# Kernel optimization log

Measured on AMD Instinct MI355X. Metric: run time of the kernel, lower is better.

The kernel has to match this reference:

```python
import jax, jax.numpy as jnp
import numpy as np

B, N, V, H, R, A, IN, K = 64, 512, 64, 512, 4, 18, 128, 32
EPS = 1e-8


def setup_inputs() -> dict:
    key = jax.random.key(0)
    ks = jax.random.split(key, 20)
    g = lambda i, shape, s=1.0: jax.random.normal(ks[i], shape, jnp.float32) * s
    u = lambda i, shape: jax.random.uniform(ks[i], shape, dtype=jnp.float32)
    cin = IN + R * V
    return dict(
        x=g(0, (B, IN)),
        h=g(1, (B, H), 0.1),
        c=g(2, (B, H), 0.1),
        memory=g(3, (B, N, V), 0.1),
        read_weights=u(4, (B, R, N)),
        write_weights=u(5, (B, N)),
        usage=u(6, (B, N)),
        link_matrix=u(7, (B, N, N)) * 0.01,
        precedence_weights=u(8, (B, N)),
        W_ih=g(9, (4 * H, cin), 0.05), W_hh=g(10, (4 * H, H), 0.05),
        b_ih=jnp.zeros(4 * H, jnp.float32), b_hh=jnp.zeros(4 * H, jnp.float32),
        W_read=g(11, (R, V + 4, H), 0.05), b_read=jnp.zeros((R, V + 4), jnp.float32),
        W_write=g(12, (3 * V + 3, H), 0.05), b_write=jnp.zeros(3 * V + 3, jnp.float32),
        W_pol=g(13, (A, H), 0.05), b_pol=jnp.zeros(A, jnp.float32),
        W_val=g(14, (1, H), 0.05), b_val=jnp.zeros(1, jnp.float32),
    )


def reference(x, h, c, memory, read_weights, write_weights, usage, link_matrix,
              precedence_weights, W_ih, W_hh, b_ih, b_hh, W_read, b_read,
              W_write, b_write, W_pol, b_pol, W_val, b_val):
    # ---- read heads (vectorized over R) ----
    ro = jnp.einsum('roh,bh->bro', W_read, h) + b_read            # [B,R,V+4]
    rkey = ro[..., :V]
    rbeta = jax.nn.softplus(ro[..., V])                           # [B,R]
    rpi = jax.nn.softmax(ro[..., V + 1:V + 4], axis=-1)           # backward/content/forward gates
    mem_norm = jnp.maximum(jnp.linalg.norm(memory, axis=-1), EPS)  # [B,N]
    key_norm = jnp.maximum(jnp.linalg.norm(rkey, axis=-1), EPS)    # [B,R]
    sim = jnp.einsum('bnv,brv->brn', memory, rkey) / (mem_norm[:, None, :] * key_norm[..., None])
    scores = rbeta[..., None] * sim                                # [B,R,N]
    kth = jax.lax.top_k(scores, K)[0][..., -1:]                    # sparse top-k mask
    cw = jax.nn.softmax(jnp.where(scores >= kth, scores, -jnp.inf), axis=-1)
    fw = jnp.einsum('bnm,brm->brn', link_matrix, read_weights)     # forward weighting L w
    bw = jnp.einsum('bmn,brm->brn', link_matrix, read_weights)     # backward weighting L^T w
    w_r = rpi[..., 0:1] * bw + rpi[..., 1:2] * cw + rpi[..., 2:3] * fw  # [B,R,N]
    rvec = jnp.einsum('brn,bnv->brv', w_r, memory).reshape(B, R * V)
    # ---- LSTM controller (torch LSTMCell gate order i,f,g,o) ----
    gates = jnp.concatenate([x, rvec], -1) @ W_ih.T + h @ W_hh.T + b_ih + b_hh
    i_g, f_g, g_g, o_g = jnp.split(gates, 4, axis=-1)
    c_new = jax.nn.sigmoid(f_g) * c + jax.nn.sigmoid(i_g) * jnp.tanh(g_g)
    h_new = jax.nn.sigmoid(o_g) * jnp.tanh(c_new)
    # ---- write head ----
    wo = h_new @ W_write.T + b_write                               # [B,3V+3]
    wkey = wo[:, :V]
    erase = jax.nn.sigmoid(wo[:, V:2 * V])
    add = jnp.tanh(wo[:, 2 * V:3 * V])
    wbeta = jax.nn.softplus(wo[:, 3 * V])
    g_a = jax.nn.sigmoid(wo[:, 3 * V + 1])
    g_w = jax.nn.sigmoid(wo[:, 3 * V + 2])
    wkey_norm = jnp.maximum(jnp.linalg.norm(wkey, axis=-1), EPS)
    wsim = jnp.einsum('bnv,bv->bn', memory, wkey) / (mem_norm * wkey_norm[:, None])
    cw_w = jax.nn.softmax(wbeta[:, None] * wsim, axis=-1)
    # allocation weighting from sorted usage (DNC Eq. 1)
    idx = jnp.argsort(usage, axis=-1)
    u_sorted = jnp.take_along_axis(usage, idx, -1)
    prod_prev = jnp.concatenate([jnp.ones((B, 1), usage.dtype), jnp.cumprod(u_sorted, -1)[:, :-1]], -1)
    a_sorted = (1.0 - u_sorted) * prod_prev
    alloc = jnp.take_along_axis(a_sorted, jnp.argsort(idx, -1), -1)
    write_w = g_w[:, None] * (g_a[:, None] * alloc + (1.0 - g_a)[:, None] * cw_w)  # [B,N]
    # ---- memory erase/add ----
    mem_new = memory * (1.0 - write_w[:, :, None] * erase[:, None, :]) + write_w[:, :, None] * add[:, None, :]
    # ---- usage (psi detached as in torch.no_grad) ----
    psi = jax.lax.stop_gradient(jnp.prod(1.0 - w_r, axis=1))
    usage_new = (usage + write_weights - usage * write_weights) * psi
    # ---- link matrix + precedence ----
    ws = jnp.sum(write_w, -1, keepdims=True)
    prec_new = (1.0 - ws) * precedence_weights + write_w
    decay = (1.0 - write_w[:, :, None]) * (1.0 - write_w[:, None, :])
    link_new = decay * link_matrix + write_w[:, :, None] * precedence_weights[:, None, :]
    link_new = link_new * (1.0 - jnp.eye(N, dtype=link_new.dtype))
    # ---- actor/critic heads ----
    logits = h_new @ W_pol.T + b_pol
    value = h_new @ W_val.T + b_val
    return (logits, value, h_new, c_new, mem_new, w_r, write_w, usage_new, link_new, prec_new)
```

## Files before the change

### kernel.cpp

```cpp
#include <hip/hip_runtime.h>
#include <math.h>

constexpr int Bb = 64, Nn = 512, Vv = 64, Hh = 512, Rr = 4, Aa = 18, INp = 128, KTOP = 32;
constexpr int CIN = 384;
constexpr int WOUT = 195;
#define EPSf 1e-8f

__device__ __forceinline__ float sigmoidf(float x){ return 1.f/(1.f+expf(-x)); }
__device__ __forceinline__ float softplusf(float x){ return (x>20.f)? x : log1pf(expf(x)); }
__device__ __forceinline__ float wave_reduce(float v){
  #pragma unroll
  for(int o=32;o>0;o>>=1) v += __shfl_down(v, o, 64);
  return v;
}
__device__ __forceinline__ unsigned f2ord(float f){
  unsigned u = __float_as_uint(f);
  return (u & 0x80000000u) ? ~u : (u | 0x80000000u);
}
__device__ __forceinline__ const float* wrow_sel(int d, const float* Ww, const float* Wp, const float* Wv){
  return (d < WOUT) ? Ww + (size_t)d*Hh : ((d < WOUT+Aa) ? Wp + (size_t)(d-WOUT)*Hh : Wv);
}

__global__ void k_stage1(const float* __restrict__ link, const float* __restrict__ rw,
                         const float* __restrict__ Wr, const float* __restrict__ brd,
                         const float* __restrict__ h, const float* __restrict__ mem,
                         float* __restrict__ fw, float* __restrict__ bwpart,
                         float* __restrict__ rvec, float* __restrict__ rp,
                         float* __restrict__ cw) {
  __shared__ __align__(16) float smem[8192];
  if (blockIdx.x < 1024) {
    float4 (*bl4)[4][128] = reinterpret_cast<float4 (*)[4][128]>(smem);
    if (blockIdx.x < 64) rvec[blockIdx.x*256 + threadIdx.x] = 0.f;
    int b  = blockIdx.x >> 4;
    int ch = blockIdx.x & 15;
    int wv = threadIdx.x >> 6, lane = threadIdx.x & 63;
    const float* rwb = rw + b*Rr*Nn;
    const float4* rw4 = (const float4*)rwb;
    float4 rwv4[4][2];
    #pragma unroll
    for (int r = 0; r < 4; ++r) {
      rwv4[r][0] = rw4[r*128 + lane];
      rwv4[r][1] = rw4[r*128 + 64 + lane];
    }
    float4 bwacc[2][4];
    #pragma unroll
    for (int t = 0; t < 2; ++t)
      #pragma unroll
      for (int r = 0; r < 4; ++r) bwacc[t][r] = make_float4(0.f,0.f,0.f,0.f);
    const float4* lb4 = (const float4*)(link + (size_t)b*Nn*Nn);
    int n0 = ch*32 + wv*8;
    #pragma unroll 2
    for (int i = 0; i < 8; ++i) {
      int n = n0 + i;
      float4 A = lb4[n*128 + lane];
      float4 Bv = lb4[n*128 + 64 + lane];
      float s0 = rwb[n], s1 = rwb[512+n], s2 = rwb[1024+n], s3 = rwb[1536+n];
      float f0 = A.x*rwv4[0][0].x + A.y*rwv4[0][0].y + A.z*rwv4[0][0].z + A.w*rwv4[0][0].w
               + Bv.x*rwv4[0][1].x + Bv.y*rwv4[0][1].y + Bv.z*rwv4[0][1].z + Bv.w*rwv4[0][1].w;
      float f1 = A.x*rwv4[1][0].x + A.y*rwv4[1][0].y + A.z*rwv4[1][0].z + A.w*rwv4[1][0].w
               + Bv.x*rwv4[1][1].x + Bv.y*rwv4[1][1].y + Bv.z*rwv4[1][1].z + Bv.w*rwv4[1][1].w;
      float f2 = A.x*rwv4[2][0].x + A.y*rwv4[2][0].y + A.z*rwv4[2][0].z + A.w*rwv4[2][0].w
               + Bv.x*rwv4[2][1].x + Bv.y*rwv4[2][1].y + Bv.z*rwv4[2][1].z + Bv.w*rwv4[2][1].w;
      float f3 = A.x*rwv4[3][0].x + A.y*rwv4[3][0].y + A.z*rwv4[3][0].z + A.w*rwv4[3][0].w
               + Bv.x*rwv4[3][1].x + Bv.y*rwv4[3][1].y + Bv.z*rwv4[3][1].z + Bv.w*rwv4[3][1].w;
      bwacc[0][0].x += A.x*s0; bwacc[0][0].y += A.y*s0; bwacc[0][0].z += A.z*s0; bwacc[0][0].w += A.w*s0;
      bwacc[0][1].x += A.x*s1; bwacc[0][1].y += A.y*s1; bwacc[0][1].z += A.z*s1; bwacc[0][1].w += A.w*s1;
      bwacc[0][2].x += A.x*s2; bwacc[0][2].y += A.y*s2; bwacc[0][2].z += A.z*s2; bwacc[0][2].w += A.w*s2;
      bwacc[0][3].x += A.x*s3; bwacc[0][3].y += A.y*s3; bwacc[0][3].z += A.z*s3; bwacc[0][3].w += A.w*s3;
      bwacc[1][0].x += Bv.x*s0; bwacc[1][0].y += Bv.y*s0; bwacc[1][0].z += Bv.z*s0; bwacc[1][0].w += Bv.w*s0;
      bwacc[1][1].x += Bv.x*s1; bwacc[1][1].y += Bv.y*s1; bwacc[1][1].z += Bv.z*s1; bwacc[1][1].w += Bv.w*s1;
      bwacc[1][2].x += Bv.x*s2; bwacc[1][2].y += Bv.y*s2; bwacc[1][2].z += Bv.z*s2; bwacc[1][2].w += Bv.w*s2;
      bwacc[1][3].x += Bv.x*s3; bwacc[1][3].y += Bv.y*s3; bwacc[1][3].z += Bv.z*s3; bwacc[1][3].w += Bv.w*s3;
      #pragma unroll
      for (int o = 32; o > 0; o >>= 1) {
        f0 += __shfl_down(f0,o,64); f1 += __shfl_down(f1,o,64);
        f2 += __shfl_down(f2,o,64); f3 += __shfl_down(f3,o,64);
      }
      if (lane == 0) {
        fw[(b*Rr+0)*Nn+n] = f0; fw[(b*Rr+1)*Nn+n] = f1;
        fw[(b*Rr+2)*Nn+n] = f2; fw[(b*Rr+3)*Nn+n] = f3;
      }
    }
    #pragma unroll
    for (int r = 0; r < 4; ++r) {
      bl4[wv][r][lane]      = bwacc[0][r];
      bl4[wv][r][64 + lane] = bwacc[1][r];
    }
    __syncthreads();
    int tid = threadIdx.x;
    float4* bwp4 = (float4*)bwpart;
    #pragma unroll
    for (int q = 0; q < 2; ++q) {
      int fid = q*256 + tid;
      int r = fid >> 7, j4 = fid & 127;
      float4 a = bl4[0][r][j4], bb = bl4[1][r][j4], cc = bl4[2][r][j4], dd = bl4[3][r][j4];
      float4 v;
      v.x = a.x+bb.x+cc.x+dd.x; v.y = a.y+bb.y+cc.y+dd.y;
      v.z = a.z+bb.z+cc.z+dd.z; v.w = a.w+bb.w+cc.w+dd.w;
      bwp4[((size_t)(ch*Bb + b)*Rr + r)*128 + j4] = v;
    }
  } else {
    float* sh  = smem;
    float* sro = smem + 512;
    unsigned long long* sk = (unsigned long long*)(smem + 592);
    float* sred = smem + 1616;
    float* skv  = smem + 1620;
    int blk = blockIdx.x - 1024;
    int b = blk >> 2, r = blk & 3;
    int tid = threadIdx.x;
    int wv = tid >> 6, lane = tid & 63;
    const float* hb = h + b*Hh;
    for (int i = tid; i < 512; i += 256) sh[i] = hb[i];
    __syncthreads();
    const float* wbase = Wr + (size_t)(r*68)*Hh;
    int pbase = wv*17;
    #pragma unroll
    for (int g = 0; g < 4; ++g) {
      int p = pbase + g*4;
      const float *w0 = wbase + (size_t)p*Hh, *w1 = w0 + Hh, *w2 = w1 + Hh, *w3 = w2 + Hh;
      float a0=0,a1=0,a2=0,a3=0;
      #pragma unroll
      for (int t = 0; t < 8; ++t) {
        int k = lane + 64*t; float hv = sh[k];
        a0 += w0[k]*hv; a1 += w1[k]*hv; a2 += w2[k]*hv; a3 += w3[k]*hv;
      }
      #pragma unroll
      for (int o = 32; o > 0; o >>= 1) {
        a0 += __shfl_down(a0,o,64); a1 += __shfl_down(a1,o,64);
        a2 += __shfl_down(a2,o,64); a3 += __shfl_down(a3,o,64);
      }
      if (lane == 0) {
        sro[p]   = a0 + brd[r*68+p];   sro[p+1] = a1 + brd[r*68+p+1];
        sro[p+2] = a2 + brd[r*68+p+2]; sro[p+3] = a3 + brd[r*68+p+3];
      }
    }
    {
      int p = pbase + 16;
      const float* w0 = wbase + (size_t)p*Hh;
      float a0 = 0.f;
      #pragma unroll
      for (int t = 0; t < 8; ++t) { int k = lane + 64*t; a0 += w0[k]*sh[k]; }
      a0 = wave_reduce(a0);
      if (lane == 0) sro[p] = a0 + brd[r*68+p];
    }
    __syncthreads();
    if (wv == 0) {
      float kv = sro[lane];
      float k2 = wave_reduce(kv*kv);
      if (lane == 0) {
        float rbeta = softplusf(sro[64]);
        float sc = rbeta / fmaxf(sqrtf(k2), EPSf);
        float e0 = sro[65], e1 = sro[66], e2 = sro[67];
        float mm = fmaxf(e0, fmaxf(e1, e2));
        float x0 = expf(e0-mm), x1 = expf(e1-mm), x2 = expf(e2-mm);
        float inv = 1.f/(x0+x1+x2);
        float* rpb = rp + (b*4 + r)*4;
        rpb[0] = sc; rpb[1] = x0*inv; rpb[2] = x1*inv; rpb[3] = x2*inv;
        sro[68] = sc;
      }
    }
    __syncthreads();
    float sc = sro[68];
    const float4* key4 = (const float4*)sro;
    float v0, v1;
    {
      const float4* m4 = (const float4*)(mem + ((size_t)(b*Nn + tid))*Vv);
      float dot=0.f, nrm=0.f;
      #pragma unroll
      for (int i = 0; i < 16; ++i) {
        float4 mv = m4[i]; float4 kk = key4[i];
        dot += mv.x*kk.x + mv.y*kk.y + mv.z*kk.z + mv.w*kk.w;
        nrm += mv.x*mv.x + mv.y*mv.y + mv.z*mv.z + mv.w*mv.w;
      }
      v0 = sc * dot / fmaxf(sqrtf(nrm), EPSf);
    }
    {
      const float4* m4 = (const float4*)(mem + ((size_t)(b*Nn + tid + 256))*Vv);
      float dot=0.f, nrm=0.f;
      #pragma unroll
      for (int i = 0; i < 16; ++i) {
        float4 mv = m4[i]; float4 kk = key4[i];
        dot += mv.x*kk.x + mv.y*kk.y + mv.z*kk.z + mv.w*kk.w;
        nrm += mv.x*mv.x + mv.y*mv.y + mv.z*mv.z + mv.w*mv.w;
      }
      v1 = sc * dot / fmaxf(sqrtf(nrm), EPSf);
    }
    unsigned long long k0 = ((unsigned long long)f2ord(v0) << 32) | (unsigned)(511 - tid);
    unsigned long long k1 = ((unsigned long long)f2ord(v1) << 32) | (unsigned)(255 - tid);
    sk[tid] = k0; sk[tid+256] = k1;
    __syncthreads();
    int c0 = 0, c1 = 0;
    #pragma unroll 8
    for (int j = 0; j < 512; ++j) {
      unsigned long long kj = sk[j];
      c0 += (kj > k0); c1 += (kj > k1);
    }
    if (c0 == KTOP-1) skv[0] = v0;
    if (c1 == KTOP-1) skv[0] = v1;
    if (c0 == 0) skv[1] = v0;
    if (c1 == 0) skv[1] = v1;
    __syncthreads();
    float kth = skv[0], mx = skv[1];
    float e0 = (v0 >= kth) ? expf(v0-mx) : 0.f;
    float e1 = (v1 >= kth) ? expf(v1-mx) : 0.f;
    float s = wave_reduce(e0+e1);
    if (lane == 0) sred[wv] = s;
    __syncthreads();
    float inv = 1.f/(sred[0]+sred[1]+sred[2]+sred[3]);
    int brr = b*4 + r;
    cw[brr*Nn+tid]     = e0*inv;
    cw[brr*Nn+tid+256] = e1*inv;
  }
}

__global__ void k_wrrv(const float* __restrict__ bwpart, const float* __restrict__ cw,
                       const float* __restrict__ fw, const float* __restrict__ rp,
                       const float* __restrict__ usage, const float* __restrict__ wwt,
                       const float* __restrict__ mem,
                       float* __restrict__ out_wr, float* __restrict__ out_usage,
                       float* __restrict__ rvec) {
  __shared__ float swr[4][64];
  int b = blockIdx.x >> 3, ch = blockIdx.x & 7;
  int tid = threadIdx.x;
  int r = tid >> 6, nl = tid & 63;
  int n = ch*64 + nl;
  int brr = b*4 + r;
  float bwv = 0.f;
  #pragma unroll
  for (int chh = 0; chh < 16; ++chh)
    bwv += bwpart[((size_t)(chh*Bb + b)*Rr + r)*Nn + n];
  const float* rpb = rp + brr*4;
  float w = rpb[1]*bwv + rpb[2]*cw[brr*Nn+n] + rpb[3]*fw[brr*Nn+n];
  out_wr[brr*Nn+n] = w;
  swr[r][nl] = w;
  __syncthreads();
  if (tid < 64) {
    int idx = b*Nn + ch*64 + tid;
    float psi = (1.f-swr[0][tid])*(1.f-swr[1][tid])*(1.f-swr[2][tid])*(1.f-swr[3][tid]);
    float u = usage[idx], wt = wwt[idx];
    out_usage[idx] = (u + wt - u*wt) * psi;
  }
  const float* mb = mem + ((size_t)b*Nn + ch*64)*Vv + nl;
  float acc = 0.f;
  #pragma unroll 16
  for (int t = 0; t < 64; ++t) acc += swr[r][t] * mb[t*Vv];
  atomicAdd(&rvec[brr*Vv + nl], acc);
}

__global__ void k_gates_lstm(const float* __restrict__ x, const float* __restrict__ rvec,
                             const float* __restrict__ h, const float* __restrict__ Wih,
                             const float* __restrict__ Whh, const float* __restrict__ bih,
                             const float* __restrict__ bhh, const float* __restrict__ c,
                             float* __restrict__ out_h, float* __restrict__ out_c) {
  int gid = blockIdx.x*4 + (threadIdx.x>>6);
  int lane = threadIdx.x & 63;
  int hh = gid >> 4;
  int bt = gid & 15;
  float acc[4][4] = {};
  #pragma unroll
  for (int t = 0; t < 6; ++t) {
    int k = lane + 64*t;
    float u[4], w[4];
    #pragma unroll
    for (int i = 0; i < 4; ++i) {
      int b = bt*4 + i;
      u[i] = (k < INp) ? x[b*INp + k] : rvec[b*(Rr*Vv) + k - INp];
      w[i] = Wih[(size_t)(i*Hh + hh)*CIN + k];
    }
    #pragma unroll
    for (int g = 0; g < 4; ++g)
      #pragma unroll
      for (int bb = 0; bb < 4; ++bb) acc[g][bb] += w[g]*u[bb];
  }
  #pragma unroll
  for (int t = 0; t < 8; ++t) {
    int k = lane + 64*t;
    float u[4], w[4];
    #pragma unroll
    for (int i = 0; i < 4; ++i) {
      u[i] = h[(bt*4+i)*Hh + k];
      w[i] = Whh[(size_t)(i*Hh + hh)*Hh + k];
    }
    #pragma unroll
    for (int g = 0; g < 4; ++g)
      #pragma unroll
      for (int bb = 0; bb < 4; ++bb) acc[g][bb] += w[g]*u[bb];
  }
  #pragma unroll
  for (int g = 0; g < 4; ++g)
    #pragma unroll
    for (int bb = 0; bb < 4; ++bb) acc[g][bb] = wave_reduce(acc[g][bb]);
  if (lane == 0) {
    float bsum[4];
    #pragma unroll
    for (int g = 0; g < 4; ++g) bsum[g] = bih[g*Hh + hh] + bhh[g*Hh + hh];
    #pragma unroll
    for (int bb = 0; bb < 4; ++bb) {
      int b = bt*4 + bb;
      float ig = sigmoidf(acc[0][bb] + bsum[0]);
      float fg = sigmoidf(acc[1][bb] + bsum[1]);
      float gg = tanhf   (acc[2][bb] + bsum[2]);
      float og = sigmoidf(acc[3][bb] + bsum[3]);
      float cn = fg * c[b*Hh + hh] + ig * gg;
      float hn = og * tanhf(cn);
      out_c[b*Hh + hh] = cn;
      out_h[b*Hh + hh] = hn;
    }
  }
}

__global__ void k_tail(const float* __restrict__ hn, const float* __restrict__ Ww,
                       const float* __restrict__ bw_, const float* __restrict__ Wp,
                       const float* __restrict__ bp, const float* __restrict__ Wv,
                       const float* __restrict__ bv, const float* __restrict__ usage,
                       const float* __restrict__ prec, const float* __restrict__ mem,
                       float* __restrict__ wo, float* __restrict__ out_logits,
                       float* __restrict__ out_value, float* __restrict__ out_ww,
                       float* __restrict__ out_prec) {
  __shared__ __align__(16) float sh[512];
  __shared__ __align__(16) float swo[200];
  __shared__ unsigned long long sk[512];
  __shared__ float su[512];
  __shared__ float cp[512];
  __shared__ float sred[8];
  int b = blockIdx.x, tid = threadIdx.x;
  int wv = tid >> 6, lane = tid & 63;
  const float* hb = hn + b*Hh;
  sh[tid] = hb[tid]; sh[tid+256] = hb[tid+256];
  __syncthreads();
  const float4* sh4 = (const float4*)sh;
  float4 h0 = sh4[lane*2], h1 = sh4[lane*2+1];
  int dbeg = wv*54, dend = (dbeg + 54 < 214) ? dbeg + 54 : 214;
  for (int p = dbeg; p < dend; p += 4) {
    int d1 = (p+1 < 213) ? p+1 : 213, d2 = (p+2 < 213) ? p+2 : 213, d3 = (p+3 < 213) ? p+3 : 213;
    const float4* w04 = (const float4*)wrow_sel(p,  Ww, Wp, Wv);
    const float4* w14 = (const float4*)wrow_sel(d1, Ww, Wp, Wv);
    const float4* w24 = (const float4*)wrow_sel(d2, Ww, Wp, Wv);
    const float4* w34 = (const float4*)wrow_sel(d3, Ww, Wp, Wv);
    float4 A0 = w04[lane*2], B0 = w04[lane*2+1];
    float4 A1 = w14[lane*2], B1 = w14[lane*2+1];
    float4 A2 = w24[lane*2], B2 = w24[lane*2+1];
    float4 A3 = w34[lane*2], B3 = w34[lane*2+1];
    float a0 = A0.x*h0.x + A0.y*h0.y + A0.z*h0.z + A0.w*h0.w
             + B0.x*h1.x + B0.y*h1.y + B0.z*h1.z + B0.w*h1.w;
    float a1 = A1.x*h0.x + A1.y*h0.y + A1.z*h0.z + A1.w*h0.w
             + B1.x*h1.x + B1.y*h1.y + B1.z*h1.z + B1.w*h1.w;
    float a2 = A2.x*h0.x + A2.y*h0.y + A2.z*h0.z + A2.w*h0.w
             + B2.x*h1.x + B2.y*h1.y + B2.z*h1.z + B2.w*h1.w;
    float a3 = A3.x*h0.x + A3.y*h0.y + A3.z*h0.z + A3.w*h0.w
             + B3.x*h1.x + B3.y*h1.y + B3.z*h1.z + B3.w*h1.w;
    #pragma unroll
    for (int o = 32; o > 0; o >>= 1) {
      a0 += __shfl_down(a0,o,64); a1 += __shfl_down(a1,o,64);
      a2 += __shfl_down(a2,o,64); a3 += __shfl_down(a3,o,64);
    }
    if (lane == 0) {
      float av[4] = {a0,a1,a2,a3};
      #pragma unroll
      for (int i = 0; i < 4; ++i) {
        int d = p + i;
        if (d >= dend) break;
        float a = av[i];
        if (d < WOUT)          { float vv = a + bw_[d]; swo[d] = vv; wo[b*WOUT+d] = vv; }
        else if (d < WOUT+Aa)  { out_logits[b*Aa + (d-WOUT)] = a + bp[d-WOUT]; }
        else                   { out_value[b] = a + bv[0]; }
      }
    }
  }
  __syncthreads();
  float wbeta = softplusf(swo[192]);
  const float4* key4 = (const float4*)swo;
  float s0, s1;
  {
    const float4* m4 = (const float4*)(mem + ((size_t)(b*Nn + tid))*Vv);
    float dot=0.f, nrm=0.f, kn=0.f;
    #pragma unroll
    for (int i = 0; i < 16; ++i) {
      float4 mv = m4[i]; float4 kk = key4[i];
      dot += mv.x*kk.x + mv.y*kk.y + mv.z*kk.z + mv.w*kk.w;
      nrm += mv.x*mv.x + mv.y*mv.y + mv.z*mv.z + mv.w*mv.w;
      kn  += kk.x*kk.x + kk.y*kk.y + kk.z*kk.z + kk.w*kk.w;
    }
    s0 = wbeta * dot / (fmaxf(sqrtf(nrm), EPSf) * fmaxf(sqrtf(kn), EPSf));
  }
  {
    const float4* m4 = (const float4*)(mem + ((size_t)(b*Nn + tid + 256))*Vv);
    float dot=0.f, nrm=0.f, kn=0.f;
    #pragma unroll
    for (int i = 0; i < 16; ++i) {
      float4 mv = m4[i]; float4 kk = key4[i];
      dot += mv.x*kk.x + mv.y*kk.y + mv.z*kk.z + mv.w*kk.w;
      nrm += mv.x*mv.x + mv.y*mv.y + mv.z*mv.z + mv.w*mv.w;
      kn  += kk.x*kk.x + kk.y*kk.y + kk.z*kk.z + kk.w*kk.w;
    }
    s1 = wbeta * dot / (fmaxf(sqrtf(nrm), EPSf) * fmaxf(sqrtf(kn), EPSf));
  }
  float u0 = usage[b*Nn+tid], u1 = usage[b*Nn+tid+256];
  unsigned long long k0 = ((unsigned long long)f2ord(u0) << 32) | (unsigned)tid;
  unsigned long long k1 = ((unsigned long long)f2ord(u1) << 32) | (unsigned)(tid+256);
  sk[tid] = k0; sk[tid+256] = k1;
  float mxl = fmaxf(s0, s1);
  #pragma unroll
  for (int o = 32; o > 0; o >>= 1) mxl = fmaxf(mxl, __shfl_down(mxl,o,64));
  if (lane == 0) sred[wv] = mxl;
  __syncthreads();
  float mx = fmaxf(fmaxf(sred[0],sred[1]), fmaxf(sred[2],sred[3]));
  float e0 = expf(s0-mx), e1 = expf(s1-mx);
  float ssum = wave_reduce(e0+e1);
  if (lane == 0) sred[4+wv] = ssum;
  int r0 = 0, r1 = 0;
  #pragma unroll 8
  for (int j = 0; j < 512; ++j) {
    unsigned long long kj = sk[j];
    r0 += (kj < k0); r1 += (kj < k1);
  }
  __syncthreads();
  float cinv = 1.f/(sred[4]+sred[5]+sred[6]+sred[7]);
  float c0 = e0*cinv, c1 = e1*cinv;
  su[r0] = u0; su[r1] = u1;
  __syncthreads();
  cp[tid] = su[tid]; cp[tid+256] = su[tid+256];
  __syncthreads();
  for (int d = 1; d < 512; d <<= 1) {
    float t0 = cp[tid]     * ((tid >= d)     ? cp[tid-d]     : 1.f);
    float t1 = cp[tid+256] * ((tid+256 >= d) ? cp[tid+256-d] : 1.f);
    __syncthreads();
    cp[tid] = t0; cp[tid+256] = t1;
    __syncthreads();
  }
  float pp0 = (r0 == 0) ? 1.f : cp[r0-1];
  float pp1 = (r1 == 0) ? 1.f : cp[r1-1];
  float a0 = (1.f-u0)*pp0, a1 = (1.f-u1)*pp1;
  float ga = sigmoidf(swo[193]);
  float gw = sigmoidf(swo[194]);
  float wv0 = gw * (ga*a0 + (1.f-ga)*c0);
  float wv1 = gw * (ga*a1 + (1.f-ga)*c1);
  out_ww[b*Nn+tid]     = wv0;
  out_ww[b*Nn+tid+256] = wv1;
  float ws_ = wave_reduce(wv0+wv1);
  if (lane == 0) sred[wv] = ws_;
  __syncthreads();
  float wsum = sred[0]+sred[1]+sred[2]+sred[3];
  out_prec[b*Nn+tid]     = (1.f-wsum)*prec[b*Nn+tid]     + wv0;
  out_prec[b*Nn+tid+256] = (1.f-wsum)*prec[b*Nn+tid+256] + wv1;
}

__global__ void k_memlink(const float* __restrict__ link, const float* __restrict__ ww,
                          const float* __restrict__ prec, const float* __restrict__ mem,
                          const float* __restrict__ wo, float* __restrict__ out_link,
                          float* __restrict__ out_mem) {
  int bid = blockIdx.x;
  if (bid < 16384) {
    int idx4 = bid*256 + threadIdx.x;
    int base = idx4*4;
    int b = base >> 18;
    int rem = base & 262143;
    int i = rem >> 9;
    int j0 = rem & 511;
    float wi = ww[b*Nn + i];
    float fi = 1.f - wi;
    float4 lv = *(const float4*)(link + base);
    float4 wj = *(const float4*)(ww + b*Nn + j0);
    float4 pj = *(const float4*)(prec + b*Nn + j0);
    float4 o;
    o.x = fi*(1.f-wj.x)*lv.x + wi*pj.x;
    o.y = fi*(1.f-wj.y)*lv.y + wi*pj.y;
    o.z = fi*(1.f-wj.z)*lv.z + wi*pj.z;
    o.w = fi*(1.f-wj.w)*lv.w + wi*pj.w;
    if (i >= j0 && i < j0+4) {
      if (i == j0) o.x = 0.f;
      else if (i == j0+1) o.y = 0.f;
      else if (i == j0+2) o.z = 0.f;
      else o.w = 0.f;
    }
    *(float4*)(out_link + base) = o;
  } else {
    int idx4 = (bid - 16384)*256 + threadIdx.x;
    int base = idx4*4;
    int b = base >> 15;
    int rem = base & 32767;
    int n = rem >> 6;
    int v0 = rem & 63;
    float w = ww[b*Nn + n];
    const float* wob = wo + b*WOUT;
    float4 m = *(const float4*)(mem + base);
    float4 o;
    float e, a;
    e = sigmoidf(wob[64+v0+0]); a = tanhf(wob[128+v0+0]); o.x = m.x*(1.f-w*e)+w*a;
    e = sigmoidf(wob[64+v0+1]); a = tanhf(wob[128+v0+1]); o.y = m.y*(1.f-w*e)+w*a;
    e = sigmoidf(wob[64+v0+2]); a = tanhf(wob[128+v0+2]); o.z = m.z*(1.f-w*e)+w*a;
    e = sigmoidf(wob[64+v0+3]); a = tanhf(wob[128+v0+3]); o.w = m.w*(1.f-w*e)+w*a;
    *(float4*)(out_mem + base) = o;
  }
}

extern "C" void kernel_launch(void* const* d_in, const int* in_sizes, int n_in,
                              void* d_out, int out_size, void* d_ws, size_t ws_size,
                              hipStream_t stream) {
  const float* x    = (const float*)d_in[0];
  const float* h    = (const float*)d_in[1];
  const float* c    = (const float*)d_in[2];
  const float* mem  = (const float*)d_in[3];
  const float* rw   = (const float*)d_in[4];
  const float* wwt  = (const float*)d_in[5];
  const float* usage= (const float*)d_in[6];
  const float* link = (const float*)d_in[7];
  const float* prec = (const float*)d_in[8];
  const float* Wih  = (const float*)d_in[9];
  const float* Whh  = (const float*)d_in[10];
  const float* bih  = (const float*)d_in[11];
  const float* bhh  = (const float*)d_in[12];
  const float* Wr   = (const float*)d_in[13];
  const float* br   = (const float*)d_in[14];
  const float* Ww   = (const float*)d_in[15];
  const float* bw_  = (const float*)d_in[16];
  const float* Wp   = (const float*)d_in[17];
  const float* bp   = (const float*)d_in[18];
  const float* Wv   = (const float*)d_in[19];
  const float* bv   = (const float*)d_in[20];

  float* out = (float*)d_out;
  float* o_logits = out + 0;
  float* o_value  = out + 1152;
  float* o_h      = out + 1216;
  float* o_c      = out + 33984;
  float* o_mem    = out + 66752;
  float* o_wr     = out + 2163904;
  float* o_ww     = out + 2294976;
  float* o_usage  = out + 2327744;
  float* o_link   = out + 2360512;
  float* o_prec   = out + 19137728;

  float* ws = (float*)d_ws;
  float* ws_rp     = ws;
  float* ws_cw     = ws + 1024;
  float* ws_fw     = ws + 132096;
  float* ws_bwpart = ws + 263168;
  float* ws_rvec   = ws + 2360320;
  float* ws_wo     = ws + 2376704;

  k_stage1     <<<dim3(1280),       dim3(256), 0, stream>>>(link, rw, Wr, br, h, mem, ws_fw, ws_bwpart, ws_rvec, ws_rp, ws_cw);
  k_wrrv       <<<dim3(Bb*8),       dim3(256), 0, stream>>>(ws_bwpart, ws_cw, ws_fw, ws_rp, usage, wwt, mem, o_wr, o_usage, ws_rvec);
  k_gates_lstm <<<dim3(2048),       dim3(256), 0, stream>>>(x, ws_rvec, h, Wih, Whh, bih, bhh, c, o_h, o_c);
  k_tail       <<<dim3(Bb),         dim3(256), 0, stream>>>(o_h, Ww, bw_, Wp, bp, Wv, bv, usage, prec, mem, ws_wo, o_logits, o_value, o_ww, o_prec);
  k_memlink    <<<dim3(16384+2048), dim3(256), 0, stream>>>(link, o_ww, prec, mem, ws_wo, o_link, o_mem);
}
```

Before: 307.3 us.

## Tile link matrix through LDS for forward/backward read weightings

Rewrites the link-matrix part of stage1 so each block loads 64x64 tiles of the link matrix into padded shared memory and computes both L·w (row dot) and Lᵀ·w (column dot) from the tile. Blocks now cover 64-row stripes (8 per batch) instead of 32-row chunks, which halves the partial backward-weight buffer and the reduction work in k_wrrv. It replaces the shuffle reductions and the large per-thread register accumulators with scalar LDS dot products, at the cost of two barriers per tile, scalar LDS stores and fewer blocks (512 versus 1024) to stream the matrix.

Result: faster. 292.5 us (-4.8%).

```diff
diff --git a/kernel.cpp b/kernel.cpp
--- a/kernel.cpp
+++ b/kernel.cpp
@@ -27,85 +27,55 @@
                          float* __restrict__ fw, float* __restrict__ bwpart,
                          float* __restrict__ rvec, float* __restrict__ rp,
                          float* __restrict__ cw) {
-  __shared__ __align__(16) float smem[8192];
-  if (blockIdx.x < 1024) {
-    float4 (*bl4)[4][128] = reinterpret_cast<float4 (*)[4][128]>(smem);
-    if (blockIdx.x < 64) rvec[blockIdx.x*256 + threadIdx.x] = 0.f;
-    int b  = blockIdx.x >> 4;
-    int ch = blockIdx.x & 15;
-    int wv = threadIdx.x >> 6, lane = threadIdx.x & 63;
-    const float* rwb = rw + b*Rr*Nn;
-    const float4* rw4 = (const float4*)rwb;
-    float4 rwv4[4][2];
-    #pragma unroll
-    for (int r = 0; r < 4; ++r) {
-      rwv4[r][0] = rw4[r*128 + lane];
-      rwv4[r][1] = rw4[r*128 + 64 + lane];
-    }
-    float4 bwacc[2][4];
-    #pragma unroll
-    for (int t = 0; t < 2; ++t)
-      #pragma unroll
-      for (int r = 0; r < 4; ++r) bwacc[t][r] = make_float4(0.f,0.f,0.f,0.f);
+  __shared__ __align__(16) float smem[6208];
+  if (blockIdx.x < 512) {
+    float* lds   = smem;
+    float* ldsrw = smem + 4160;
+    int b  = blockIdx.x >> 3;
+    int st = blockIdx.x & 7;
+    int tid = threadIdx.x;
+    {
+      const float4* rw4 = (const float4*)(rw + b*Rr*Nn);
+      float4* lrw4 = (float4*)ldsrw;
+      lrw4[tid] = rw4[tid];
+      lrw4[tid+256] = rw4[tid+256];
+    }
+    if (blockIdx.x < 64) rvec[blockIdx.x*256 + tid] = 0.f;
+    __syncthreads();
+    int row = tid & 63, rr = tid >> 6;
+    float facc = 0.f;
     const float4* lb4 = (const float4*)(link + (size_t)b*Nn*Nn);
-    int n0 = ch*32 + wv*8;
-    #pragma unroll 2
-    for (int i = 0; i < 8; ++i) {
-      int n = n0 + i;
-      float4 A = lb4[n*128 + lane];
-      float4 Bv = lb4[n*128 + 64 + lane];
-      float s0 = rwb[n], s1 = rwb[512+n], s2 = rwb[1024+n], s3 = rwb[1536+n];
-      float f0 = A.x*rwv4[0][0].x + A.y*rwv4[0][0].y + A.z*rwv4[0][0].z + A.w*rwv4[0][0].w
-               + Bv.x*rwv4[0][1].x + Bv.y*rwv4[0][1].y + Bv.z*rwv4[0][1].z + Bv.w*rwv4[0][1].w;
-      float f1 = A.x*rwv4[1][0].x + A.y*rwv4[1][0].y + A.z*rwv4[1][0].z + A.w*rwv4[1][0].w
-               + Bv.x*rwv4[1][1].x + Bv.y*rwv4[1][1].y + Bv.z*rwv4[1][1].z + Bv.w*rwv4[1][1].w;
-      float f2 = A.x*rwv4[2][0].x + A.y*rwv4[2][0].y + A.z*rwv4[2][0].z + A.w*rwv4[2][0].w
-               + Bv.x*rwv4[2][1].x + Bv.y*rwv4[2][1].y + Bv.z*rwv4[2][1].z + Bv.w*rwv4[2][1].w;
-      float f3 = A.x*rwv4[3][0].x + A.y*rwv4[3][0].y + A.z*rwv4[3][0].z + A.w*rwv4[3][0].w
-               + Bv.x*rwv4[3][1].x + Bv.y*rwv4[3][1].y + Bv.z*rwv4[3][1].z + Bv.w*rwv4[3][1].w;
-      bwacc[0][0].x += A.x*s0; bwacc[0][0].y += A.y*s0; bwacc[0][0].z += A.z*s0; bwacc[0][0].w += A.w*s0;
-      bwacc[0][1].x += A.x*s1; bwacc[0][1].y += A.y*s1; bwacc[0][1].z += A.z*s1; bwacc[0][1].w += A.w*s1;
-      bwacc[0][2].x += A.x*s2; bwacc[0][2].y += A.y*s2; bwacc[0][2].z += A.z*s2; bwacc[0][2].w += A.w*s2;
-      bwacc[0][3].x += A.x*s3; bwacc[0][3].y += A.y*s3; bwacc[0][3].z += A.z*s3; bwacc[0][3].w += A.w*s3;
-      bwacc[1][0].x += Bv.x*s0; bwacc[1][0].y += Bv.y*s0; bwacc[1][0].z += Bv.z*s0; bwacc[1][0].w += Bv.w*s0;
-      bwacc[1][1].x += Bv.x*s1; bwacc[1][1].y += Bv.y*s1; bwacc[1][1].z += Bv.z*s1; bwacc[1][1].w += Bv.w*s1;
-      bwacc[1][2].x += Bv.x*s2; bwacc[1][2].y += Bv.y*s2; bwacc[1][2].z += Bv.z*s2; bwacc[1][2].w += Bv.w*s2;
-      bwacc[1][3].x += Bv.x*s3; bwacc[1][3].y += Bv.y*s3; bwacc[1][3].z += Bv.z*s3; bwacc[1][3].w += Bv.w*s3;
-      #pragma unroll
-      for (int o = 32; o > 0; o >>= 1) {
-        f0 += __shfl_down(f0,o,64); f1 += __shfl_down(f1,o,64);
-        f2 += __shfl_down(f2,o,64); f3 += __shfl_down(f3,o,64);
-      }
-      if (lane == 0) {
-        fw[(b*Rr+0)*Nn+n] = f0; fw[(b*Rr+1)*Nn+n] = f1;
-        fw[(b*Rr+2)*Nn+n] = f2; fw[(b*Rr+3)*Nn+n] = f3;
-      }
-    }
-    #pragma unroll
-    for (int r = 0; r < 4; ++r) {
-      bl4[wv][r][lane]      = bwacc[0][r];
-      bl4[wv][r][64 + lane] = bwacc[1][r];
-    }
-    __syncthreads();
-    int tid = threadIdx.x;
-    float4* bwp4 = (float4*)bwpart;
-    #pragma unroll
-    for (int q = 0; q < 2; ++q) {
-      int fid = q*256 + tid;
-      int r = fid >> 7, j4 = fid & 127;
-      float4 a = bl4[0][r][j4], bb = bl4[1][r][j4], cc = bl4[2][r][j4], dd = bl4[3][r][j4];
-      float4 v;
-      v.x = a.x+bb.x+cc.x+dd.x; v.y = a.y+bb.y+cc.y+dd.y;
-      v.z = a.z+bb.z+cc.z+dd.z; v.w = a.w+bb.w+cc.w+dd.w;
-      bwp4[((size_t)(ch*Bb + b)*Rr + r)*128 + j4] = v;
-    }
+    const float* rwn = ldsrw + rr*512 + st*64;
+    for (int jt = 0; jt < 8; ++jt) {
+      #pragma unroll
+      for (int q = 0; q < 4; ++q) {
+        int idx4 = tid*4 + q;
+        int tr = idx4 >> 4;
+        int c4 = idx4 & 15;
+        float4 v = lb4[(size_t)(st*64 + tr)*128 + jt*16 + c4];
+        int base = tr*65 + c4*4;
+        lds[base] = v.x; lds[base+1] = v.y; lds[base+2] = v.z; lds[base+3] = v.w;
+      }
+      __syncthreads();
+      const float* rwj = ldsrw + rr*512 + jt*64;
+      float a = 0.f;
+      #pragma unroll 8
+      for (int j = 0; j < 64; ++j) a += lds[row*65 + j] * rwj[j];
+      facc += a;
+      float bacc = 0.f;
+      #pragma unroll 8
+      for (int n = 0; n < 64; ++n) bacc += lds[n*65 + row] * rwn[n];
+      bwpart[((size_t)(st*Bb + b)*Rr + rr)*Nn + jt*64 + row] = bacc;
+      __syncthreads();
+    }
+    fw[(b*Rr + rr)*Nn + st*64 + row] = facc;
   } else {
     float* sh  = smem;
     float* sro = smem + 512;
     unsigned long long* sk = (unsigned long long*)(smem + 592);
     float* sred = smem + 1616;
     float* skv  = smem + 1620;
-    int blk = blockIdx.x - 1024;
+    int blk = blockIdx.x - 512;
     int b = blk >> 2, r = blk & 3;
     int tid = threadIdx.x;
     int wv = tid >> 6, lane = tid & 63;
@@ -227,7 +197,7 @@
   int brr = b*4 + r;
   float bwv = 0.f;
   #pragma unroll
-  for (int chh = 0; chh < 16; ++chh)
+  for (int chh = 0; chh < 8; ++chh)
     bwv += bwpart[((size_t)(chh*Bb + b)*Rr + r)*Nn + n];
   const float* rpb = rp + brr*4;
   float w = rpb[1]*bwv + rpb[2]*cw[brr*Nn+n] + rpb[3]*fw[brr*Nn+n];
@@ -536,10 +506,10 @@
   float* ws_cw     = ws + 1024;
   float* ws_fw     = ws + 132096;
   float* ws_bwpart = ws + 263168;
-  float* ws_rvec   = ws + 2360320;
-  float* ws_wo     = ws + 2376704;
-
-  k_stage1     <<<dim3(1280),       dim3(256), 0, stream>>>(link, rw, Wr, br, h, mem, ws_fw, ws_bwpart, ws_rvec, ws_rp, ws_cw);
+  float* ws_rvec   = ws + 1311744;
+  float* ws_wo     = ws + 1328128;
+
+  k_stage1     <<<dim3(768),        dim3(256), 0, stream>>>(link, rw, Wr, br, h, mem, ws_fw, ws_bwpart, ws_rvec, ws_rp, ws_cw);
   k_wrrv       <<<dim3(Bb*8),       dim3(256), 0, stream>>>(ws_bwpart, ws_cw, ws_fw, ws_rp, usage, wwt, mem, o_wr, o_usage, ws_rvec);
   k_gates_lstm <<<dim3(2048),       dim3(256), 0, stream>>>(x, ws_rvec, h, Wih, Whh, bih, bhh, c, o_h, o_c);
   k_tail       <<<dim3(Bb),         dim3(256), 0, stream>>>(o_h, Ww, bw_, Wp, bp, Wv, bv, usage, prec, mem, ws_wo, o_logits, o_value, o_ww, o_prec);
```
